# Performance work log

Measured on AMD Instinct MI355X. Metric: run time of the kernel, lower is better.

Reference implementation:

```python
import jax, jax.numpy as jnp
import numpy as np

B = 16; V = 30522; D = 512; H = 8; DH = 64; FF = 2048
NC = 4; NF = 30; NN = 34; FL = 64; HL = 32; NLAYERS = 2

def _pos_encoding(L, d):
    pos = np.arange(L)[:, None].astype(np.float32)
    i = np.arange(0, d, 2)[None, :].astype(np.float32)
    ang = pos / np.power(10000.0, i / d)
    pe = np.zeros((L, d), dtype=np.float32)
    pe[:, 0::2] = np.sin(ang)
    pe[:, 1::2] = np.cos(ang)
    return jnp.asarray(pe)

def _ln(x, g, b):
    m = x.mean(-1, keepdims=True)
    v = ((x - m) ** 2).mean(-1, keepdims=True)
    return (x - m) / jnp.sqrt(v + 1e-5) * g + b

def _encoder(ids, emb, Wqkv, bqkv, Wo, bo, ln1_g, ln1_b, Wff1, bff1, Wff2, bff2, ln2_g, ln2_b):
    Bx, L = ids.shape
    x = emb[ids] * jnp.sqrt(jnp.float32(D)) + _pos_encoding(L, D)
    for l in range(NLAYERS):  # torch post-norm encoder layer, relu FFN
        qkv = x @ Wqkv[l] + bqkv[l]
        q, k, v = jnp.split(qkv, 3, axis=-1)
        q = q.reshape(Bx, L, H, DH); k = k.reshape(Bx, L, H, DH); v = v.reshape(Bx, L, H, DH)
        att = jax.nn.softmax(jnp.einsum('blhd,bmhd->bhlm', q, k) / jnp.sqrt(jnp.float32(DH)), axis=-1)
        o = jnp.einsum('bhlm,bmhd->blhd', att, v).reshape(Bx, L, D) @ Wo[l] + bo[l]
        x = _ln(x + o, ln1_g[l], ln1_b[l])
        f = jax.nn.relu(x @ Wff1[l] + bff1[l]) @ Wff2[l] + bff2[l]
        x = _ln(x + f, ln2_g[l], ln2_b[l])
    return x

def _masked_mean(emb, mask):
    m = mask[..., None]
    return (emb * m).sum(1) / jnp.clip(m.sum(1), 1e-9, None)

def _solve_edges(W, adj, iters=100, lr=0.05, c=10.0):
    # differentiable proxy for the CvxpyLayer SDP relaxation: projected gradient
    # ascent on symmetric E in [0,1], maximizing sum(W*E) with quadratic penalties
    # for sum(adj*E) <= 6 and trace(E[:4,:4]) == 1 (PSD constraint dropped).
    diag4 = jnp.zeros((NN, NN)).at[jnp.arange(NC), jnp.arange(NC)].set(1.0)
    E0 = jnp.full(W.shape, 0.5)
    def step(E, _):
        s = jnp.sum(adj * E, axis=(1, 2), keepdims=True)
        d = jnp.sum(E * diag4, axis=(1, 2), keepdims=True)
        g = W - 2.0 * c * jax.nn.relu(s - 6.0) * adj - 2.0 * c * (d - 1.0) * diag4
        En = E + lr * g
        En = jnp.clip(0.5 * (En + jnp.swapaxes(En, 1, 2)), 0.0, 1.0)
        return En, None
    E, _ = jax.lax.scan(step, E0, None, length=iters)
    return E

def setup_inputs():
    key = jax.random.key(0)
    ks = jax.random.split(key, 24)
    w = lambda k, shape: (jax.random.normal(k, shape) * 0.02).astype(jnp.float32)
    return {
        'hypothesis_input_ids': jax.random.randint(ks[0], (B, NC, HL), 0, V),
        'hypothesis_attention_mask': jnp.ones((B, NC, HL), jnp.float32),
        'fact_attention_mask': jnp.ones((B, NF, FL), jnp.float32),
        'fact_input_ids': jax.random.randint(ks[1], (B, NF, FL), 0, V),
        'grounding_grounding_overlap': jax.random.uniform(ks[2], (B, NN, NN)),
        'abstract_abstract_overlap': jax.random.uniform(ks[3], (B, NN, NN)),
        'abstract_abstract_similarity': jax.random.uniform(ks[4], (B, NN, NN)),
        'question_grounding_overlap': jax.random.uniform(ks[5], (B, NN, NN)),
        'question_abstract_overlap': jax.random.uniform(ks[6], (B, NN, NN)),
        'question_abstract_similarity': jax.random.uniform(ks[7], (B, NN, NN)),
        'grounding_abstract_overlap': jax.random.uniform(ks[8], (B, NN, NN)),
        'question_question_score': w(ks[9], (B, NN, NN)),
        'labels': jax.random.randint(ks[10], (B,), 0, NC),
        'gold_similarity_scores': jax.random.normal(ks[11], (B, NC, NF)),
        'emb_table': w(ks[12], (V, D)),
        'Wqkv': w(ks[13], (NLAYERS, D, 3 * D)), 'bqkv': jnp.zeros((NLAYERS, 3 * D)),
        'Wo': w(ks[14], (NLAYERS, D, D)), 'bo': jnp.zeros((NLAYERS, D)),
        'ln1_g': jnp.ones((NLAYERS, D)), 'ln1_b': jnp.zeros((NLAYERS, D)),
        'Wff1': w(ks[15], (NLAYERS, D, FF)), 'bff1': jnp.zeros((NLAYERS, FF)),
        'Wff2': w(ks[16], (NLAYERS, FF, D)), 'bff2': jnp.zeros((NLAYERS, D)),
        'ln2_g': jnp.ones((NLAYERS, D)), 'ln2_b': jnp.zeros((NLAYERS, D)),
        'score_W': w(ks[17], (4 * D,)), 'score_b': jnp.zeros(()),
        'abs_score_W': w(ks[18], (4 * D,)), 'abs_score_b': jnp.zeros(()),
        'p_aa_overlap': jnp.ones(()), 'p_aa_sim': jnp.ones(()),
        'p_qa_overlap': jnp.ones(()), 'p_qa_sim': jnp.ones(()),
    }

def reference(hypothesis_input_ids, hypothesis_attention_mask, fact_attention_mask, fact_input_ids,
              grounding_grounding_overlap, abstract_abstract_overlap, abstract_abstract_similarity,
              question_grounding_overlap, question_abstract_overlap, question_abstract_similarity,
              grounding_abstract_overlap, question_question_score, labels, gold_similarity_scores,
              emb_table, Wqkv, bqkv, Wo, bo, ln1_g, ln1_b, Wff1, bff1, Wff2, bff2, ln2_g, ln2_b,
              score_W, score_b, abs_score_W, abs_score_b, p_aa_overlap, p_aa_sim, p_qa_overlap, p_qa_sim):
    enc = lambda ids: _encoder(ids, emb_table, Wqkv, bqkv, Wo, bo, ln1_g, ln1_b,
                               Wff1, bff1, Wff2, bff2, ln2_g, ln2_b)
    fseq = _masked_mean(enc(fact_input_ids.reshape(-1, FL)),
                        fact_attention_mask.reshape(-1, FL)).reshape(-1, NF, D)
    hseq = _masked_mean(enc(hypothesis_input_ids.reshape(-1, HL)),
                        hypothesis_attention_mask.reshape(-1, HL)).reshape(-1, NC, D)
    # abstract-abstract pairwise: concat(f_j, f_i, |f_j-f_i|, f_j*f_i) @ abs_score_W, done chunk-wise
    A1, A2, A3, A4 = jnp.split(abs_score_W, 4)
    aa = (fseq @ A1)[:, None, :] + (fseq @ A2)[:, :, None] \
       + jnp.einsum('bijd,d->bij', jnp.abs(fseq[:, None, :, :] - fseq[:, :, None, :]), A3) \
       + jnp.einsum('bid,bjd->bij', fseq * A4, fseq) + abs_score_b
    aa_sm = jax.nn.softmax(aa.reshape(-1, NF * NF), axis=1).reshape(-1, NF, NF)
    aa_sm = aa_sm * (1.0 - jnp.eye(NF))  # zero diagonal
    aa_sim = abstract_abstract_similarity.at[:, NC:, NC:].set(aa_sm)
    # question-abstract pairwise: concat(f_k, h_c, |f_k-h_c|, f_k*h_c) @ score_W
    S1, S2, S3, S4 = jnp.split(score_W, 4)
    qa = (fseq @ S1)[:, None, :] + (hseq @ S2)[:, :, None] \
       + jnp.einsum('bckd,d->bck', jnp.abs(fseq[:, None, :, :] - hseq[:, :, None, :]), S3) \
       + jnp.einsum('bkd,bcd->bck', fseq * S4, hseq) + score_b
    similarity_scores = jax.nn.softmax(qa, axis=2)  # [B, NC, NF]
    qa_sim = jnp.zeros_like(grounding_abstract_overlap)
    qa_sim = qa_sim.at[:, NC:, :NC].set(jnp.transpose(similarity_scores, (0, 2, 1)))
    qa_sim = qa_sim.at[:, :NC, NC:].set(similarity_scores)
    edge_weights = (-p_aa_overlap * abstract_abstract_overlap + p_aa_sim * aa_sim
                    + p_qa_overlap * question_abstract_overlap + p_qa_sim * qa_sim
                    + question_question_score)
    adj = (edge_weights != 0).astype(jnp.float32)
    edges = _solve_edges(edge_weights, adj)
    final_pred = jnp.diagonal(edges[:, :NC, :NC], axis1=1, axis2=2)  # [B, NC]
    gold = jax.nn.softmax(gold_similarity_scores, axis=2)
    logp = jax.nn.log_softmax(final_pred, axis=1)
    ce = -jnp.mean(logp[jnp.arange(final_pred.shape[0]), labels])
    mse = jnp.mean((similarity_scores - gold) ** 2)
    return ce + mse, final_pred
```

## Files before the change

kernel.cpp:

```cpp
#include <hip/hip_runtime.h>
#include <cstdint>
#include <cstddef>


using u16 = unsigned short;

typedef __bf16 bf16x8 __attribute__((ext_vector_type(8)));
typedef float  floatx4 __attribute__((ext_vector_type(4)));

#if defined(__has_builtin)
#if __has_builtin(__builtin_amdgcn_global_load_lds)
#define USE_GLL 1
#endif
#endif

__device__ __forceinline__ float bf2f(u16 u) {
  return __uint_as_float(((unsigned)u) << 16);
}
__device__ __forceinline__ u16 f2bf(float f) {
  unsigned u = __float_as_uint(f);
  u += 0x7FFFu + ((u >> 16) & 1u);
  return (u16)(u >> 16);
}
__device__ __forceinline__ float ldf(const void* p, size_t i, int isb) {
  return isb ? bf2f(((const u16*)p)[i]) : ((const float*)p)[i];
}

__device__ __forceinline__ float waveSum(float v) {
#pragma unroll
  for (int o = 32; o > 0; o >>= 1) v += __shfl_xor(v, o, 64);
  return v;
}
__device__ __forceinline__ float waveMax(float v) {
#pragma unroll
  for (int o = 32; o > 0; o >>= 1) v = fmaxf(v, __shfl_xor(v, o, 64));
  return v;
}
__device__ __forceinline__ float blockSum(float v, float* sh4) {
  v = waveSum(v);
  if ((threadIdx.x & 63) == 0) sh4[threadIdx.x >> 6] = v;
  __syncthreads();
  float r = sh4[0] + sh4[1] + sh4[2] + sh4[3];
  __syncthreads();
  return r;
}
__device__ __forceinline__ float blockMax(float v, float* sh4) {
  v = waveMax(v);
  if ((threadIdx.x & 63) == 0) sh4[threadIdx.x >> 6] = v;
  __syncthreads();
  float r = fmaxf(fmaxf(sh4[0], sh4[1]), fmaxf(sh4[2], sh4[3]));
  __syncthreads();
  return r;
}

__global__ void detect_kernel(const void* __restrict__ ln1g, int* __restrict__ flag) {
  unsigned u = *(const unsigned*)ln1g;
  *flag = (u == 0x3F800000u) ? 0 : 1;
}

__global__ __launch_bounds__(256) void pe_kernel(float* __restrict__ petab) {
  const int pos = blockIdx.x;
  const float LOG1E4_OVER_D = 9.210340371976184f / 512.0f;
  for (int d = threadIdx.x; d < 512; d += 256) {
    int i2 = d & ~1;
    float ang = (float)pos * expf(-(float)i2 * LOG1E4_OVER_D);
    petab[pos * 512 + d] = (d & 1) ? cosf(ang) : sinf(ang);
  }
}

__global__ __launch_bounds__(256) void transpose_kernel(const void* __restrict__ src,
                                                        u16* __restrict__ dst,
                                                        int K, int N,
                                                        size_t srcz, size_t dstz,
                                                        const int* __restrict__ F) {
  const int isb = *F;
  __shared__ u16 tile[32][33];
  size_t eoff = (size_t)blockIdx.z * srcz;
  u16* d = dst + (size_t)blockIdx.z * dstz;
  int bx = blockIdx.x, by = blockIdx.y;
  int tx = threadIdx.x & 31, ty = threadIdx.x >> 5;
  for (int i = ty; i < 32; i += 8)
    tile[i][tx] = f2bf(ldf(src, eoff + (size_t)(by * 32 + i) * N + bx * 32 + tx, isb));
  __syncthreads();
  for (int i = ty; i < 32; i += 8)
    d[(size_t)(bx * 32 + i) * K + by * 32 + tx] = tile[tx][i];
}

__global__ __launch_bounds__(256) void embed_kernel(const int* __restrict__ ids,
                                                    const void* __restrict__ emb,
                                                    u16* __restrict__ x, int L,
                                                    const float* __restrict__ petab,
                                                    const int* __restrict__ F) {
  const int isb = *F;
  int tok = blockIdx.x;
  int pos = tok % L;
  int id = ids[tok];
  for (int d = threadIdx.x; d < 512; d += 256) {
    float e = ldf(emb, (size_t)id * 512 + d, isb) * 22.62741699796952f;
    x[(size_t)tok * 512 + d] = f2bf(e + petab[pos * 512 + d]);
  }
}

__global__ __launch_bounds__(256) void embed2_kernel(const int* __restrict__ fids,
                                                     const int* __restrict__ hids,
                                                     const void* __restrict__ emb,
                                                     u16* __restrict__ x,
                                                     const float* __restrict__ petab,
                                                     const int* __restrict__ F) {
  const int isb = *F;
  int tok = blockIdx.x;
  int id, pos;
  if (tok < 30720) { id = fids[tok]; pos = tok & 63; }
  else             { int t2 = tok - 30720; id = hids[t2]; pos = t2 & 31; }
  for (int d = threadIdx.x; d < 512; d += 256) {
    float e = ldf(emb, (size_t)id * 512 + d, isb) * 22.62741699796952f;
    x[(size_t)tok * 512 + d] = f2bf(e + petab[pos * 512 + d]);
  }
}

template <int RELU>
__global__ __launch_bounds__(256, 2) void gemm_bt(const u16* __restrict__ A,
                                                  const u16* __restrict__ Bt,
                                                  const void* __restrict__ bias,
                                                  u16* __restrict__ C,
                                                  int M, int N, int K, size_t boff,
                                                  const int* __restrict__ F) {
  const int isb = *F;
  __shared__ __align__(16) u16 As[128 * 64];
  __shared__ __align__(16) u16 Bs[128 * 64];
  const int tid = threadIdx.x;
  const int lane = tid & 63;
  const int wave = tid >> 6;
  const int wm = wave >> 1, wn = wave & 1;
  const int l15 = lane & 15, quad = lane >> 4;

  const int nwg = gridDim.x * gridDim.y;
  const int hw  = blockIdx.y * gridDim.x + blockIdx.x;
  int lg;
  if ((nwg & 7) == 0) {
    lg = (hw & 7) * (nwg >> 3) + (hw >> 3);
  } else {
    int q = nwg >> 3, r = nwg & 7;
    int xcd = hw & 7, j = hw >> 3;
    lg = (xcd < r ? xcd * (q + 1) : r * (q + 1) + (xcd - r) * q) + j;
  }
  const int bm = lg / gridDim.x;
  const int bn = lg - bm * gridDim.x;

  floatx4 acc[4][4];
#pragma unroll
  for (int i = 0; i < 4; i++)
#pragma unroll
    for (int j = 0; j < 4; j++) acc[i][j] = (floatx4){0.f, 0.f, 0.f, 0.f};

  const u16* Abase = A + (size_t)bm * 128 * K;
  const u16* Bbase = Bt + (size_t)bn * 128 * K;

  for (int kt = 0; kt < K; kt += 64) {
#pragma unroll
    for (int i = 0; i < 4; i++) {
      int c = i * 256 + tid;
      int row = c >> 3, p = c & 7;
      int col = (((p - row) & 7)) * 8;
      const u16* ga = &Abase[(size_t)row * K + kt + col];
      const u16* gb = &Bbase[(size_t)row * K + kt + col];
#ifdef USE_GLL
      __builtin_amdgcn_global_load_lds(
          (const __attribute__((address_space(1))) void*)ga,
          (__attribute__((address_space(3))) void*)&As[c * 8], 16, 0, 0);
      __builtin_amdgcn_global_load_lds(
          (const __attribute__((address_space(1))) void*)gb,
          (__attribute__((address_space(3))) void*)&Bs[c * 8], 16, 0, 0);
#else
      *(uint4*)&As[c * 8] = *(const uint4*)ga;
      *(uint4*)&Bs[c * 8] = *(const uint4*)gb;
#endif
    }
    __syncthreads();
#pragma unroll
    for (int ks = 0; ks < 2; ks++) {
      bf16x8 af[4], bfr[4];
#pragma unroll
      for (int mi = 0; mi < 4; mi++) {
        int ra = wm * 64 + mi * 16 + l15;
        int q = ks * 4 + quad;
        af[mi] = *(const bf16x8*)&As[ra * 64 + ((q + ra) & 7) * 8];
      }
#pragma unroll
      for (int ni = 0; ni < 4; ni++) {
        int rb = wn * 64 + ni * 16 + l15;
        int q = ks * 4 + quad;
        bfr[ni] = *(const bf16x8*)&Bs[rb * 64 + ((q + rb) & 7) * 8];
      }
#pragma unroll
      for (int mi = 0; mi < 4; mi++)
#pragma unroll
        for (int ni = 0; ni < 4; ni++)
          acc[mi][ni] = __builtin_amdgcn_mfma_f32_16x16x32_bf16(af[mi], bfr[ni], acc[mi][ni], 0, 0, 0);
    }
    __syncthreads();
  }

  float bv[4];
  const int gcb = bn * 128 + wn * 64 + l15;
#pragma unroll
  for (int ni = 0; ni < 4; ni++) bv[ni] = ldf(bias, boff + gcb + ni * 16, isb);
#pragma unroll
  for (int mi = 0; mi < 4; mi++) {
#pragma unroll
    for (int r = 0; r < 4; r++) {
      int grow = bm * 128 + wm * 64 + mi * 16 + quad * 4 + r;
      size_t rb = (size_t)grow * N + gcb;
#pragma unroll
      for (int ni = 0; ni < 4; ni++) {
        float v = acc[mi][ni][r] + bv[ni];
        if (RELU) v = fmaxf(v, 0.f);
        C[rb + ni * 16] = f2bf(v);
      }
    }
  }
}

__global__ __launch_bounds__(256) void attn_kernel(const u16* __restrict__ qkv,
                                                   u16* __restrict__ o, int L,
                                                   int nblk1,
                                                   const u16* __restrict__ qkv2,
                                                   u16* __restrict__ o2, int L2) {
  int bid = blockIdx.x;
  if (bid >= nblk1) { qkv = qkv2; o = o2; L = L2; bid -= nblk1; }
  const int h = bid & 7;
  const int s = bid >> 3;
  __shared__ __align__(16) u16 Qs[64 * 72];
  __shared__ __align__(16) u16 Ks[64 * 72];
  __shared__ __align__(16) u16 Vt[64 * 72];
  __shared__ float Ss[64 * 66];
  const int tid = threadIdx.x;
  const int lane = tid & 63;
  const int wave = tid >> 6;
  const int wm = wave >> 1, wn = wave & 1;
  const int l15 = lane & 15, quad = lane >> 4;
  const int base = s * L;

  for (int idx = tid; idx < 512; idx += 256) {
    int t = idx >> 3, d8 = (idx & 7) * 8;
    int rot = ((t >> 3) + (idx & 7)) & 7;
    if (t < L) {
      size_t g = (size_t)(base + t) * 1536 + h * 64 + d8;
      *(uint4*)&Qs[t * 72 + d8] = *(const uint4*)&qkv[g];
      *(uint4*)&Ks[t * 72 + d8] = *(const uint4*)&qkv[g + 512];
      u16 vv[8];
      *(uint4*)vv = *(const uint4*)&qkv[g + 1024];
#pragma unroll
      for (int i = 0; i < 8; i++) Vt[(d8 + i) * 72 + rot * 8 + (t & 7)] = vv[i];
    } else {
      uint4 z = {0u, 0u, 0u, 0u};
      *(uint4*)&Qs[t * 72 + d8] = z;
      *(uint4*)&Ks[t * 72 + d8] = z;
#pragma unroll
      for (int i = 0; i < 8; i++) Vt[(d8 + i) * 72 + rot * 8 + (t & 7)] = 0;
    }
  }
  __syncthreads();

  {
    floatx4 acc[2][2];
#pragma unroll
    for (int mi = 0; mi < 2; mi++)
#pragma unroll
      for (int ni = 0; ni < 2; ni++) acc[mi][ni] = (floatx4){0.f, 0.f, 0.f, 0.f};
#pragma unroll
    for (int ks = 0; ks < 2; ks++) {
      bf16x8 af[2], bfr[2];
#pragma unroll
      for (int mi = 0; mi < 2; mi++)
        af[mi] = *(const bf16x8*)&Qs[(wm * 32 + mi * 16 + l15) * 72 + ks * 32 + quad * 8];
#pragma unroll
      for (int ni = 0; ni < 2; ni++)
        bfr[ni] = *(const bf16x8*)&Ks[(wn * 32 + ni * 16 + l15) * 72 + ks * 32 + quad * 8];
#pragma unroll
      for (int mi = 0; mi < 2; mi++)
#pragma unroll
        for (int ni = 0; ni < 2; ni++)
          acc[mi][ni] = __builtin_amdgcn_mfma_f32_16x16x32_bf16(af[mi], bfr[ni], acc[mi][ni], 0, 0, 0);
    }
#pragma unroll
    for (int mi = 0; mi < 2; mi++)
#pragma unroll
      for (int ni = 0; ni < 2; ni++)
#pragma unroll
        for (int r = 0; r < 4; r++)
          Ss[(wm * 32 + mi * 16 + quad * 4 + r) * 66 + wn * 32 + ni * 16 + l15] =
              acc[mi][ni][r] * 0.125f;
  }
  __syncthreads();

  {
    int r = tid >> 2, sub = tid & 3;
    int j0 = sub * 16;
    float mx = -3.4e38f;
    if (r < L)
      for (int j = j0; j < j0 + 16; j++)
        if (j < L) mx = fmaxf(mx, Ss[r * 66 + j]);
    mx = fmaxf(mx, __shfl_xor(mx, 1, 64));
    mx = fmaxf(mx, __shfl_xor(mx, 2, 64));
    float sum = 0.f;
    if (r < L)
      for (int j = j0; j < j0 + 16; j++)
        if (j < L) { float e = expf(Ss[r * 66 + j] - mx); Ss[r * 66 + j] = e; sum += e; }
    sum += __shfl_xor(sum, 1, 64);
    sum += __shfl_xor(sum, 2, 64);
    float inv = 1.f / sum;
    if (r < L)
      for (int j = j0; j < j0 + 16; j++)
        Qs[r * 72 + j] = (j < L) ? f2bf(Ss[r * 66 + j] * inv) : (u16)0;
  }
  __syncthreads();

  {
    floatx4 acc[2][2];
#pragma unroll
    for (int mi = 0; mi < 2; mi++)
#pragma unroll
      for (int ni = 0; ni < 2; ni++) acc[mi][ni] = (floatx4){0.f, 0.f, 0.f, 0.f};
#pragma unroll
    for (int ks = 0; ks < 2; ks++) {
      bf16x8 af[2], bfr[2];
#pragma unroll
      for (int mi = 0; mi < 2; mi++)
        af[mi] = *(const bf16x8*)&Qs[(wm * 32 + mi * 16 + l15) * 72 + ks * 32 + quad * 8];
#pragma unroll
      for (int ni = 0; ni < 2; ni++) {
        int rb = wn * 32 + ni * 16 + l15;
        int p = ((ks * 4 + quad) + (rb >> 3)) & 7;
        bfr[ni] = *(const bf16x8*)&Vt[rb * 72 + p * 8];
      }
#pragma unroll
      for (int mi = 0; mi < 2; mi++)
#pragma unroll
        for (int ni = 0; ni < 2; ni++)
          acc[mi][ni] = __builtin_amdgcn_mfma_f32_16x16x32_bf16(af[mi], bfr[ni], acc[mi][ni], 0, 0, 0);
    }
#pragma unroll
    for (int mi = 0; mi < 2; mi++) {
#pragma unroll
      for (int r = 0; r < 4; r++) {
        int t = wm * 32 + mi * 16 + quad * 4 + r;
        if (t < L) {
#pragma unroll
          for (int ni = 0; ni < 2; ni++) {
            int d = wn * 32 + ni * 16 + l15;
            o[(size_t)(base + t) * 512 + h * 64 + d] = f2bf(acc[mi][ni][r]);
          }
        }
      }
    }
  }
}

__global__ __launch_bounds__(256) void add_ln_kernel(u16* __restrict__ x,
                                                     const u16* __restrict__ y,
                                                     const void* __restrict__ g,
                                                     const void* __restrict__ b,
                                                     size_t eoff,
                                                     const int* __restrict__ F) {
  const int isb = *F;
  const int row = blockIdx.x, tid = threadIdx.x;
  __shared__ float sh[4];
  size_t o0 = (size_t)row * 512 + tid * 2;
  unsigned xv = *(const unsigned*)&x[o0];
  unsigned yv = *(const unsigned*)&y[o0];
  float v0 = bf2f((u16)xv) + bf2f((u16)yv);
  float v1 = bf2f((u16)(xv >> 16)) + bf2f((u16)(yv >> 16));
  float mean = blockSum(v0 + v1, sh) * (1.f / 512.f);
  float d0 = v0 - mean, d1 = v1 - mean;
  float var = blockSum(d0 * d0 + d1 * d1, sh) * (1.f / 512.f);
  float rstd = rsqrtf(var + 1e-5f);
  float g0 = ldf(g, eoff + tid * 2, isb),     g1 = ldf(g, eoff + tid * 2 + 1, isb);
  float b0 = ldf(b, eoff + tid * 2, isb),     b1 = ldf(b, eoff + tid * 2 + 1, isb);
  unsigned r0 = f2bf(d0 * rstd * g0 + b0);
  unsigned r1 = f2bf(d1 * rstd * g1 + b1);
  *(unsigned*)&x[o0] = r0 | (r1 << 16);
}

__global__ __launch_bounds__(256) void pool_kernel(const u16* __restrict__ x,
                                                   const void* __restrict__ mask,
                                                   float* __restrict__ pooled, int L,
                                                   size_t moff,
                                                   const int* __restrict__ F) {
  const int isb = *F;
  const int s = blockIdx.x;
  float msum = 0.f;
  for (int t = 0; t < L; t++) msum += ldf(mask, moff + s * L + t, isb);
  float inv = 1.f / fmaxf(msum, 1e-9f);
  for (int d = threadIdx.x; d < 512; d += 256) {
    float acc = 0.f;
    for (int t = 0; t < L; t++)
      acc += bf2f(x[(size_t)(s * L + t) * 512 + d]) * ldf(mask, moff + s * L + t, isb);
    pooled[(size_t)s * 512 + d] = acc * inv;
  }
}

__global__ __launch_bounds__(256) void pool2_kernel(const u16* __restrict__ xf,
                                                    const void* __restrict__ fmask,
                                                    float* __restrict__ fpool,
                                                    const u16* __restrict__ xh,
                                                    const void* __restrict__ hmask,
                                                    float* __restrict__ hpool,
                                                    const int* __restrict__ F) {
  const int isb = *F;
  const u16* x; const void* mask; float* pooled; int L, s;
  if (blockIdx.x < 480) { x = xf; mask = fmask; pooled = fpool; L = 64; s = blockIdx.x; }
  else                  { x = xh; mask = hmask; pooled = hpool; L = 32; s = blockIdx.x - 480; }
  float msum = 0.f;
  for (int t = 0; t < L; t++) msum += ldf(mask, (size_t)s * L + t, isb);
  float inv = 1.f / fmaxf(msum, 1e-9f);
  for (int d = threadIdx.x; d < 512; d += 256) {
    float acc = 0.f;
    for (int t = 0; t < L; t++)
      acc += bf2f(x[(size_t)(s * L + t) * 512 + d]) * ldf(mask, (size_t)s * L + t, isb);
    pooled[(size_t)s * 512 + d] = acc * inv;
  }
}

__global__ __launch_bounds__(64) void pair2_kernel(const float* __restrict__ FS,
                                                   const float* __restrict__ HS,
                                                   const void* __restrict__ absW,
                                                   const void* __restrict__ absB,
                                                   const void* __restrict__ scW,
                                                   const void* __restrict__ scB,
                                                   float* __restrict__ AA,
                                                   float* __restrict__ QA,
                                                   const int* __restrict__ F) {
  const int isb = *F;
  int gid = blockIdx.x;
  const float *X, *Y; const void *Wv, *bs; float* outp; int NI, NJ;
  if (gid < 14400) { X = FS; Y = FS; Wv = absW; bs = absB; outp = AA; NI = 30; NJ = 30; }
  else { gid -= 14400; X = HS; Y = FS; Wv = scW; bs = scB; outp = QA; NI = 4; NJ = 30; }
  int j = gid % NJ;
  int t = gid / NJ;
  int i = t % NI;
  int b = t / NI;
  const float* xv = X + ((size_t)b * NI + i) * 512;
  const float* yv = Y + ((size_t)b * NJ + j) * 512;
  int l = threadIdx.x;
  float p = 0.f;
  for (int d = l; d < 512; d += 64) {
    float xi = xv[d], yj = yv[d];
    p += ldf(Wv, d, isb) * yj + ldf(Wv, 512 + d, isb) * xi +
         ldf(Wv, 1024 + d, isb) * fabsf(yj - xi) + ldf(Wv, 1536 + d, isb) * xi * yj;
  }
  p = waveSum(p);
  if (l == 0) outp[gid] = p + ldf(bs, 0, isb);
}

__global__ __launch_bounds__(256) void sm2_kernel(const float* __restrict__ aa,
                                                  float* __restrict__ aasm,
                                                  const float* __restrict__ qa,
                                                  float* __restrict__ sim) {
  __shared__ float sh[4];
  if (blockIdx.x < 16) {
    const int b = blockIdx.x;
    const float* src = aa + (size_t)b * 900;
    float* dst = aasm + (size_t)b * 900;
    int tid = threadIdx.x;
    float mx = -3.4e38f;
    for (int i = tid; i < 900; i += 256) mx = fmaxf(mx, src[i]);
    mx = blockMax(mx, sh);
    float sum = 0.f;
    for (int i = tid; i < 900; i += 256) sum += expf(src[i] - mx);
    sum = blockSum(sum, sh);
    float inv = 1.f / sum;
    for (int i = tid; i < 900; i += 256) {
      int r = i / 30, c = i - r * 30;
      dst[i] = (r == c) ? 0.f : expf(src[i] - mx) * inv;
    }
  } else {
    int g = (blockIdx.x - 16) * 4 + (threadIdx.x >> 6);
    int l = threadIdx.x & 63;
    float v = (l < 30) ? qa[(size_t)g * 30 + l] : -3.4e38f;
    float mx = waveMax(v);
    float e = (l < 30) ? expf(v - mx) : 0.f;
    float s = waveSum(e);
    if (l < 30) sim[(size_t)g * 30 + l] = e / s;
  }
}

__global__ __launch_bounds__(256) void edgew_kernel(const void* __restrict__ aaov,
                                                    const void* __restrict__ aasim_in,
                                                    const void* __restrict__ qaov,
                                                    const void* __restrict__ qq,
                                                    const float* __restrict__ aasm,
                                                    const float* __restrict__ sim,
                                                    const void* __restrict__ p1,
                                                    const void* __restrict__ p2,
                                                    const void* __restrict__ p3,
                                                    const void* __restrict__ p4,
                                                    float* __restrict__ Wout,
                                                    const int* __restrict__ F) {
  const int isb = *F;
  int e = blockIdx.x * 256 + threadIdx.x;
  if (e >= 16 * 1156) return;
  int b = e / 1156;
  int rem = e - b * 1156;
  int r = rem / 34, c = rem - r * 34;
  float aas;
  if (r >= 4 && c >= 4) aas = aasm[(size_t)b * 900 + (r - 4) * 30 + (c - 4)];
  else                  aas = ldf(aasim_in, e, isb);
  float qas = 0.f;
  if (r >= 4 && c < 4)      qas = sim[((size_t)b * 4 + c) * 30 + (r - 4)];
  else if (r < 4 && c >= 4) qas = sim[((size_t)b * 4 + r) * 30 + (c - 4)];
  float w = -ldf(p1, 0, isb) * ldf(aaov, e, isb) + ldf(p2, 0, isb) * aas +
            ldf(p3, 0, isb) * ldf(qaov, e, isb) + ldf(p4, 0, isb) * qas +
            ldf(qq, e, isb);
  Wout[e] = w;
}

__global__ __launch_bounds__(64) void solve_kernel(const float* __restrict__ Wmat,
                                                   float* __restrict__ pred,
                                                   float* __restrict__ outp) {
  const int b = blockIdx.x;
  const int lane = threadIdx.x;
  float E[19], Ws[19], As[19];
  bool dg[19];
#pragma unroll
  for (int k = 0; k < 19; k++) {
    int e = lane + (k << 6);
    if (e < 1156) {
      int r = e / 34, c = e - r * 34;
      float w1 = Wmat[(size_t)b * 1156 + e];
      float w2 = Wmat[(size_t)b * 1156 + c * 34 + r];
      Ws[k] = 0.5f * (w1 + w2);
      As[k] = 0.5f * (((w1 != 0.f) ? 1.f : 0.f) + ((w2 != 0.f) ? 1.f : 0.f));
      dg[k] = (r == c && r < 4);
      E[k] = 0.5f;
    } else {
      Ws[k] = 0.f; As[k] = 0.f; dg[k] = false; E[k] = 0.f;
    }
  }
  for (int it = 0; it < 100; it++) {
    float ps = 0.f;
#pragma unroll
    for (int k = 0; k < 19; k++) ps += As[k] * E[k];
    float s = waveSum(ps);
    float dd = __shfl(E[0], 0, 64) + __shfl(E[0], 35, 64) +
               __shfl(E[1], 6, 64) + __shfl(E[1], 41, 64);
    float coef_s = (s > 6.f) ? 20.f * (s - 6.f) : 0.f;
    float coef_d = 20.f * (dd - 1.f);
#pragma unroll
    for (int k = 0; k < 19; k++) {
      float g = Ws[k] - coef_s * As[k] - (dg[k] ? coef_d : 0.f);
      E[k] = fminf(fmaxf(E[k] + 0.05f * g, 0.f), 1.f);
    }
  }
  float v0 = E[0], v1 = E[1];
  if (lane == 0)  { pred[b * 4 + 0] = v0; outp[1 + b * 4 + 0] = v0; }
  if (lane == 35) { pred[b * 4 + 1] = v0; outp[1 + b * 4 + 1] = v0; }
  if (lane == 6)  { pred[b * 4 + 2] = v1; outp[1 + b * 4 + 2] = v1; }
  if (lane == 41) { pred[b * 4 + 3] = v1; outp[1 + b * 4 + 3] = v1; }
}

__global__ __launch_bounds__(256) void loss_kernel(const float* __restrict__ sim,
                                                   const void* __restrict__ gold,
                                                   const float* __restrict__ pred,
                                                   const int* __restrict__ labels,
                                                   float* __restrict__ outp,
                                                   const int* __restrict__ F) {
  const int isb = *F;
  __shared__ float sh[4];
  const int tid = threadIdx.x;
  float local = 0.f;
  if (tid < 64) {
    float mx = -3.4e38f;
    for (int k = 0; k < 30; k++) mx = fmaxf(mx, ldf(gold, (size_t)tid * 30 + k, isb));
    float sum = 0.f;
    for (int k = 0; k < 30; k++) sum += expf(ldf(gold, (size_t)tid * 30 + k, isb) - mx);
    float inv = 1.f / sum;
    for (int k = 0; k < 30; k++) {
      float gsm = expf(ldf(gold, (size_t)tid * 30 + k, isb) - mx) * inv;
      float d = sim[(size_t)tid * 30 + k] - gsm;
      local += d * d;
    }
  }
  float mse = blockSum(local, sh) * (1.f / 1920.f);
  float cel = 0.f;
  if (tid < 16) {
    const float* f = pred + tid * 4;
    int lb = labels[tid] & 3;
    float mx = fmaxf(fmaxf(f[0], f[1]), fmaxf(f[2], f[3]));
    float lse = logf(expf(f[0] - mx) + expf(f[1] - mx) + expf(f[2] - mx) + expf(f[3] - mx));
    float lp = f[lb] - mx - lse;
    cel = -lp * (1.f / 16.f);
  }
  float ce = blockSum(cel, sh);
  if (tid == 0) outp[0] = ce + mse;
}

extern "C" void kernel_launch(void* const* d_in, const int* in_sizes, int n_in,
                              void* d_out, int out_size, void* d_ws, size_t ws_size,
                              hipStream_t stream) {
  (void)in_sizes; (void)n_in; (void)out_size;
  const int*  hyp_ids   = (const int*)d_in[0];
  const void* hyp_mask  = d_in[1];
  const void* fact_mask = d_in[2];
  const int*  fact_ids  = (const int*)d_in[3];
  const void* aa_ov     = d_in[5];
  const void* aa_sim_in = d_in[6];
  const void* qa_ov     = d_in[8];
  const void* qq        = d_in[11];
  const int*  labels    = (const int*)d_in[12];
  const void* gold      = d_in[13];
  const void* emb       = d_in[14];
  const void* Wqkv      = d_in[15];
  const void* bqkv      = d_in[16];
  const void* Wo        = d_in[17];
  const void* bo        = d_in[18];
  const void* ln1g      = d_in[19];
  const void* ln1b      = d_in[20];
  const void* Wff1      = d_in[21];
  const void* bff1      = d_in[22];
  const void* Wff2      = d_in[23];
  const void* bff2      = d_in[24];
  const void* ln2g      = d_in[25];
  const void* ln2b      = d_in[26];
  const void* scoreW    = d_in[27];
  const void* scoreB    = d_in[28];
  const void* absW      = d_in[29];
  const void* absB      = d_in[30];
  const void* p_aaov    = d_in[31];
  const void* p_aasim   = d_in[32];
  const void* p_qaov    = d_in[33];
  const void* p_qasim   = d_in[34];
  float* out = (float*)d_out;

  char* ws = (char*)d_ws;
  size_t off = 0;
  auto alloc = [&](size_t bytes) -> void* {
    void* p = ws + off;
    off += (bytes + 255) & ~(size_t)255;
    return p;
  };

  float* PRED = (float*)alloc(64ull * 4);
  int*   FLAG = (int*)alloc(256);
  float* SIM  = (float*)alloc(16ull * 120 * 4);
  float* QA   = (float*)alloc(16ull * 120 * 4);
  float* AASM = (float*)alloc(16ull * 900 * 4);
  float* AA   = (float*)alloc(16ull * 900 * 4);
  float* WMAT = (float*)alloc(16ull * 1156 * 4);
  float* FSEQ = (float*)alloc(480ull * 512 * 4);
  float* HSEQ = (float*)alloc(64ull * 512 * 4);
  float* PETAB= (float*)alloc(64ull * 512 * 4);
  u16* WT_QKV = (u16*)alloc(2ull * 1536 * 512 * 2);
  u16* WT_O   = (u16*)alloc(2ull * 512 * 512 * 2);
  u16* WT_F1  = (u16*)alloc(2ull * 2048 * 512 * 2);
  u16* WT_F2  = (u16*)alloc(2ull * 512 * 2048 * 2);

  const int opts_tok[6] = {32768, 30720, 15360, 10240, 6144, 3072};
  const int opts_nch[6] = {1, 1, 2, 3, 5, 10};
  int CH_TOK = 3072, NCH = 10;
  for (int i = 0; i < 6; i++) {
    size_t need = off + (size_t)opts_tok[i] * 7168 + 4096;
    if (need <= ws_size) { CH_TOK = opts_tok[i]; NCH = opts_nch[i]; break; }
  }
  u16* X   = (u16*)alloc((size_t)CH_TOK * 512 * 2);
  u16* BIG = (u16*)alloc((size_t)CH_TOK * 2048 * 2);
  u16* ATT = (u16*)alloc((size_t)CH_TOK * 512 * 2);
  u16* Y   = (u16*)alloc((size_t)CH_TOK * 512 * 2);

  detect_kernel<<<1, 1, 0, stream>>>(ln1g, FLAG);
  pe_kernel<<<64, 256, 0, stream>>>(PETAB);

  transpose_kernel<<<dim3(48, 16, 2), 256, 0, stream>>>(
      Wqkv, WT_QKV, 512, 1536, 512ull * 1536, 1536ull * 512, FLAG);
  transpose_kernel<<<dim3(16, 16, 2), 256, 0, stream>>>(
      Wo, WT_O, 512, 512, 512ull * 512, 512ull * 512, FLAG);
  transpose_kernel<<<dim3(64, 16, 2), 256, 0, stream>>>(
      Wff1, WT_F1, 512, 2048, 512ull * 2048, 2048ull * 512, FLAG);
  transpose_kernel<<<dim3(16, 64, 2), 256, 0, stream>>>(
      Wff2, WT_F2, 2048, 512, 2048ull * 512, 512ull * 2048, FLAG);

  if (CH_TOK >= 32768) {
    const int M = 32768;
    const size_t HOFF = 30720;
    embed2_kernel<<<M, 256, 0, stream>>>(fact_ids, hyp_ids, emb, X, PETAB, FLAG);
    for (int l = 0; l < 2; l++) {
      gemm_bt<0><<<dim3(12, M / 128), 256, 0, stream>>>(
          X, WT_QKV + (size_t)l * 1536 * 512, bqkv, BIG, M, 1536, 512,
          (size_t)l * 1536, FLAG);
      attn_kernel<<<480 * 8 + 64 * 8, 256, 0, stream>>>(
          BIG, ATT, 64, 480 * 8, BIG + HOFF * 1536, ATT + HOFF * 512, 32);
      gemm_bt<0><<<dim3(4, M / 128), 256, 0, stream>>>(
          ATT, WT_O + (size_t)l * 512 * 512, bo, Y, M, 512, 512,
          (size_t)l * 512, FLAG);
      add_ln_kernel<<<M, 256, 0, stream>>>(X, Y, ln1g, ln1b, (size_t)l * 512, FLAG);
      gemm_bt<1><<<dim3(16, M / 128), 256, 0, stream>>>(
          X, WT_F1 + (size_t)l * 2048 * 512, bff1, BIG, M, 2048, 512,
          (size_t)l * 2048, FLAG);
      gemm_bt<0><<<dim3(4, M / 128), 256, 0, stream>>>(
          BIG, WT_F2 + (size_t)l * 512 * 2048, bff2, Y, M, 512, 2048,
          (size_t)l * 512, FLAG);
      add_ln_kernel<<<M, 256, 0, stream>>>(X, Y, ln2g, ln2b, (size_t)l * 512, FLAG);
    }
    pool2_kernel<<<544, 256, 0, stream>>>(X, fact_mask, FSEQ,
                                          X + HOFF * 512, hyp_mask, HSEQ, FLAG);
  } else {
    auto encode = [&](const int* ids, int nseq, int L, const void* mask,
                      size_t moff, float* pooled) {
      int M = nseq * L;
      embed_kernel<<<M, 256, 0, stream>>>(ids, emb, X, L, PETAB, FLAG);
      for (int l = 0; l < 2; l++) {
        gemm_bt<0><<<dim3(12, M / 128), 256, 0, stream>>>(
            X, WT_QKV + (size_t)l * 1536 * 512, bqkv, BIG, M, 1536, 512,
            (size_t)l * 1536, FLAG);
        attn_kernel<<<nseq * 8, 256, 0, stream>>>(BIG, ATT, L, nseq * 8, BIG, ATT, L);
        gemm_bt<0><<<dim3(4, M / 128), 256, 0, stream>>>(
            ATT, WT_O + (size_t)l * 512 * 512, bo, Y, M, 512, 512,
            (size_t)l * 512, FLAG);
        add_ln_kernel<<<M, 256, 0, stream>>>(X, Y, ln1g, ln1b, (size_t)l * 512, FLAG);
        gemm_bt<1><<<dim3(16, M / 128), 256, 0, stream>>>(
            X, WT_F1 + (size_t)l * 2048 * 512, bff1, BIG, M, 2048, 512,
            (size_t)l * 2048, FLAG);
        gemm_bt<0><<<dim3(4, M / 128), 256, 0, stream>>>(
            BIG, WT_F2 + (size_t)l * 512 * 2048, bff2, Y, M, 512, 2048,
            (size_t)l * 512, FLAG);
        add_ln_kernel<<<M, 256, 0, stream>>>(X, Y, ln2g, ln2b, (size_t)l * 512, FLAG);
      }
      pool_kernel<<<nseq, 256, 0, stream>>>(X, mask, pooled, L, moff, FLAG);
    };
    const int seq_per = 480 / NCH;
    for (int c = 0; c < NCH; c++) {
      encode(fact_ids + (size_t)c * seq_per * 64, seq_per, 64, fact_mask,
             (size_t)c * seq_per * 64, FSEQ + (size_t)c * seq_per * 512);
    }
    encode(hyp_ids, 64, 32, hyp_mask, 0, HSEQ);
  }

  pair2_kernel<<<16 * 30 * 30 + 16 * 4 * 30, 64, 0, stream>>>(
      FSEQ, HSEQ, absW, absB, scoreW, scoreB, AA, QA, FLAG);
  sm2_kernel<<<32, 256, 0, stream>>>(AA, AASM, QA, SIM);

  edgew_kernel<<<(16 * 1156 + 255) / 256, 256, 0, stream>>>(
      aa_ov, aa_sim_in, qa_ov, qq, AASM, SIM, p_aaov, p_aasim, p_qaov, p_qasim,
      WMAT, FLAG);
  solve_kernel<<<16, 64, 0, stream>>>(WMAT, PRED, out);
  loss_kernel<<<1, 256, 0, stream>>>(SIM, gold, PRED, labels, out, FLAG);
}
```

Baseline: 990.1 us.

## Fuse setup kernels into one launch and keep attention softmax in registers

Merges the dtype detect, positional-encoding, and four weight-transpose launches into a single setup kernel that dispatches on block index, cutting five kernel launches. In the attention kernel, softmax is now computed directly on the MFMA accumulators using cross-lane shuffles plus small shared row-stat arrays. This replaces the round trip through a float score buffer in shared memory. The change lowers LDS traffic and footprint, which may raise occupancy, at the cost of two extra block barriers and more live registers.

```diff
diff --git a/kernel.cpp b/kernel.cpp
--- a/kernel.cpp
+++ b/kernel.cpp
@@ -53,31 +53,51 @@
   return r;
 }
 
-__global__ void detect_kernel(const void* __restrict__ ln1g, int* __restrict__ flag) {
-  unsigned u = *(const unsigned*)ln1g;
-  *flag = (u == 0x3F800000u) ? 0 : 1;
-}
-
-__global__ __launch_bounds__(256) void pe_kernel(float* __restrict__ petab) {
-  const int pos = blockIdx.x;
-  const float LOG1E4_OVER_D = 9.210340371976184f / 512.0f;
-  for (int d = threadIdx.x; d < 512; d += 256) {
-    int i2 = d & ~1;
-    float ang = (float)pos * expf(-(float)i2 * LOG1E4_OVER_D);
-    petab[pos * 512 + d] = (d & 1) ? cosf(ang) : sinf(ang);
-  }
-}
-
-__global__ __launch_bounds__(256) void transpose_kernel(const void* __restrict__ src,
-                                                        u16* __restrict__ dst,
-                                                        int K, int N,
-                                                        size_t srcz, size_t dstz,
-                                                        const int* __restrict__ F) {
-  const int isb = *F;
+__global__ __launch_bounds__(256) void setup_kernel(const void* __restrict__ Wqkv,
+                                                    const void* __restrict__ Wo,
+                                                    const void* __restrict__ Wff1,
+                                                    const void* __restrict__ Wff2,
+                                                    u16* __restrict__ WT_QKV,
+                                                    u16* __restrict__ WT_O,
+                                                    u16* __restrict__ WT_F1,
+                                                    u16* __restrict__ WT_F2,
+                                                    float* __restrict__ petab,
+                                                    const void* __restrict__ ln1g,
+                                                    int* __restrict__ flag) {
+  const int bid = blockIdx.x;
+  unsigned u0 = *(const unsigned*)ln1g;
+  const int isb = (u0 == 0x3F800000u) ? 0 : 1;
+  if (bid == 0 && threadIdx.x == 0) *flag = isb;
+
+  if (bid >= 6144) {
+    int pos = bid - 6144;
+    const float LOG1E4_OVER_D = 9.210340371976184f / 512.0f;
+    for (int d = threadIdx.x; d < 512; d += 256) {
+      int i2 = d & ~1;
+      float ang = (float)pos * expf(-(float)i2 * LOG1E4_OVER_D);
+      petab[pos * 512 + d] = (d & 1) ? cosf(ang) : sinf(ang);
+    }
+    return;
+  }
+
+  const void* src; u16* dst; int K, N, bx, by, z;
+  if (bid < 1536) {
+    src = Wqkv; dst = WT_QKV; K = 512; N = 1536;
+    z = bid / 768; int r = bid % 768; bx = r % 48; by = r / 48;
+  } else if (bid < 2048) {
+    src = Wo; dst = WT_O; K = 512; N = 512;
+    int t = bid - 1536; z = t / 256; int r = t % 256; bx = r % 16; by = r / 16;
+  } else if (bid < 4096) {
+    src = Wff1; dst = WT_F1; K = 512; N = 2048;
+    int t = bid - 2048; z = t / 1024; int r = t % 1024; bx = r % 64; by = r / 64;
+  } else {
+    src = Wff2; dst = WT_F2; K = 2048; N = 512;
+    int t = bid - 4096; z = t / 1024; int r = t % 1024; bx = r % 16; by = r / 16;
+  }
+  size_t plane = (size_t)K * N;
+  size_t eoff = (size_t)z * plane;
+  u16* d = dst + (size_t)z * plane;
   __shared__ u16 tile[32][33];
-  size_t eoff = (size_t)blockIdx.z * srcz;
-  u16* d = dst + (size_t)blockIdx.z * dstz;
-  int bx = blockIdx.x, by = blockIdx.y;
   int tx = threadIdx.x & 31, ty = threadIdx.x >> 5;
   for (int i = ty; i < 32; i += 8)
     tile[i][tx] = f2bf(ldf(src, eoff + (size_t)(by * 32 + i) * N + bx * 32 + tx, isb));
@@ -233,7 +253,8 @@
   __shared__ __align__(16) u16 Qs[64 * 72];
   __shared__ __align__(16) u16 Ks[64 * 72];
   __shared__ __align__(16) u16 Vt[64 * 72];
-  __shared__ float Ss[64 * 66];
+  __shared__ float rstatM[64][2];
+  __shared__ float rstatS[64][2];
   const int tid = threadIdx.x;
   const int lane = tid & 63;
   const int wave = tid >> 6;
@@ -262,57 +283,100 @@
   }
   __syncthreads();
 
+  floatx4 sacc[2][2];
+#pragma unroll
+  for (int mi = 0; mi < 2; mi++)
+#pragma unroll
+    for (int ni = 0; ni < 2; ni++) sacc[mi][ni] = (floatx4){0.f, 0.f, 0.f, 0.f};
+#pragma unroll
+  for (int ks = 0; ks < 2; ks++) {
+    bf16x8 af[2], bfr[2];
+#pragma unroll
+    for (int mi = 0; mi < 2; mi++)
+      af[mi] = *(const bf16x8*)&Qs[(wm * 32 + mi * 16 + l15) * 72 + ks * 32 + quad * 8];
+#pragma unroll
+    for (int ni = 0; ni < 2; ni++)
+      bfr[ni] = *(const bf16x8*)&Ks[(wn * 32 + ni * 16 + l15) * 72 + ks * 32 + quad * 8];
+#pragma unroll
+    for (int mi = 0; mi < 2; mi++)
+#pragma unroll
+      for (int ni = 0; ni < 2; ni++)
+        sacc[mi][ni] = __builtin_amdgcn_mfma_f32_16x16x32_bf16(af[mi], bfr[ni], sacc[mi][ni], 0, 0, 0);
+  }
+
   {
-    floatx4 acc[2][2];
+    const int c0ok = (wn * 32 + l15) < L;
+    const int c1ok = (wn * 32 + 16 + l15) < L;
+    float pm[2][4];
 #pragma unroll
     for (int mi = 0; mi < 2; mi++)
 #pragma unroll
-      for (int ni = 0; ni < 2; ni++) acc[mi][ni] = (floatx4){0.f, 0.f, 0.f, 0.f};
-#pragma unroll
-    for (int ks = 0; ks < 2; ks++) {
-      bf16x8 af[2], bfr[2];
+      for (int r = 0; r < 4; r++) {
+        float a = c0ok ? sacc[mi][0][r] * 0.125f : -3.4e38f;
+        float c = c1ok ? sacc[mi][1][r] * 0.125f : -3.4e38f;
+        pm[mi][r] = fmaxf(a, c);
+      }
+#pragma unroll
+    for (int off = 1; off <= 8; off <<= 1)
 #pragma unroll
       for (int mi = 0; mi < 2; mi++)
-        af[mi] = *(const bf16x8*)&Qs[(wm * 32 + mi * 16 + l15) * 72 + ks * 32 + quad * 8];
-#pragma unroll
-      for (int ni = 0; ni < 2; ni++)
-        bfr[ni] = *(const bf16x8*)&Ks[(wn * 32 + ni * 16 + l15) * 72 + ks * 32 + quad * 8];
+#pragma unroll
+        for (int r = 0; r < 4; r++)
+          pm[mi][r] = fmaxf(pm[mi][r], __shfl_xor(pm[mi][r], off, 64));
+    if (l15 == 0) {
 #pragma unroll
       for (int mi = 0; mi < 2; mi++)
 #pragma unroll
+        for (int r = 0; r < 4; r++)
+          rstatM[wm * 32 + mi * 16 + quad * 4 + r][wn] = pm[mi][r];
+    }
+    __syncthreads();
+
+    float mx[2][4];
+#pragma unroll
+    for (int mi = 0; mi < 2; mi++)
+#pragma unroll
+      for (int r = 0; r < 4; r++) {
+        int row = wm * 32 + mi * 16 + quad * 4 + r;
+        mx[mi][r] = fmaxf(rstatM[row][0], rstatM[row][1]);
+      }
+    float ev[2][2][4];
+    float ps[2][4];
+#pragma unroll
+    for (int mi = 0; mi < 2; mi++)
+#pragma unroll
+      for (int r = 0; r < 4; r++) {
+        float e0 = c0ok ? expf(sacc[mi][0][r] * 0.125f - mx[mi][r]) : 0.f;
+        float e1 = c1ok ? expf(sacc[mi][1][r] * 0.125f - mx[mi][r]) : 0.f;
+        ev[mi][0][r] = e0; ev[mi][1][r] = e1;
+        ps[mi][r] = e0 + e1;
+      }
+#pragma unroll
+    for (int off = 1; off <= 8; off <<= 1)
+#pragma unroll
+      for (int mi = 0; mi < 2; mi++)
+#pragma unroll
+        for (int r = 0; r < 4; r++)
+          ps[mi][r] += __shfl_xor(ps[mi][r], off, 64);
+    if (l15 == 0) {
+#pragma unroll
+      for (int mi = 0; mi < 2; mi++)
+#pragma unroll
+        for (int r = 0; r < 4; r++)
+          rstatS[wm * 32 + mi * 16 + quad * 4 + r][wn] = ps[mi][r];
+    }
+    __syncthreads();
+
+#pragma unroll
+    for (int mi = 0; mi < 2; mi++)
+#pragma unroll
+      for (int r = 0; r < 4; r++) {
+        int row = wm * 32 + mi * 16 + quad * 4 + r;
+        float inv = 1.f / (rstatS[row][0] + rstatS[row][1]);
+#pragma unroll
         for (int ni = 0; ni < 2; ni++)
-          acc[mi][ni] = __builtin_amdgcn_mfma_f32_16x16x32_bf16(af[mi], bfr[ni], acc[mi][ni], 0, 0, 0);
-    }
-#pragma unroll
-    for (int mi = 0; mi < 2; mi++)
-#pragma unroll
-      for (int ni = 0; ni < 2; ni++)
-#pragma unroll
-        for (int r = 0; r < 4; r++)
-          Ss[(wm * 32 + mi * 16 + quad * 4 + r) * 66 + wn * 32 + ni * 16 + l15] =
-              acc[mi][ni][r] * 0.125f;
-  }
-  __syncthreads();
-
-  {
-    int r = tid >> 2, sub = tid & 3;
-    int j0 = sub * 16;
-    float mx = -3.4e38f;
-    if (r < L)
-      for (int j = j0; j < j0 + 16; j++)
-        if (j < L) mx = fmaxf(mx, Ss[r * 66 + j]);
-    mx = fmaxf(mx, __shfl_xor(mx, 1, 64));
-    mx = fmaxf(mx, __shfl_xor(mx, 2, 64));
-    float sum = 0.f;
-    if (r < L)
-      for (int j = j0; j < j0 + 16; j++)
-        if (j < L) { float e = expf(Ss[r * 66 + j] - mx); Ss[r * 66 + j] = e; sum += e; }
-    sum += __shfl_xor(sum, 1, 64);
-    sum += __shfl_xor(sum, 2, 64);
-    float inv = 1.f / sum;
-    if (r < L)
-      for (int j = j0; j < j0 + 16; j++)
-        Qs[r * 72 + j] = (j < L) ? f2bf(Ss[r * 66 + j] * inv) : (u16)0;
+          Qs[row * 72 + wn * 32 + ni * 16 + l15] = f2bf(ev[mi][ni][r] * inv);
+      }
   }
   __syncthreads();
 
@@ -667,17 +731,9 @@
   u16* ATT = (u16*)alloc((size_t)CH_TOK * 512 * 2);
   u16* Y   = (u16*)alloc((size_t)CH_TOK * 512 * 2);
 
-  detect_kernel<<<1, 1, 0, stream>>>(ln1g, FLAG);
-  pe_kernel<<<64, 256, 0, stream>>>(PETAB);
-
-  transpose_kernel<<<dim3(48, 16, 2), 256, 0, stream>>>(
-      Wqkv, WT_QKV, 512, 1536, 512ull * 1536, 1536ull * 512, FLAG);
-  transpose_kernel<<<dim3(16, 16, 2), 256, 0, stream>>>(
-      Wo, WT_O, 512, 512, 512ull * 512, 512ull * 512, FLAG);
-  transpose_kernel<<<dim3(64, 16, 2), 256, 0, stream>>>(
-      Wff1, WT_F1, 512, 2048, 512ull * 2048, 2048ull * 512, FLAG);
-  transpose_kernel<<<dim3(16, 64, 2), 256, 0, stream>>>(
-      Wff2, WT_F2, 2048, 512, 2048ull * 512, 512ull * 2048, FLAG);
+  setup_kernel<<<6208, 256, 0, stream>>>(Wqkv, Wo, Wff1, Wff2,
+                                         WT_QKV, WT_O, WT_F1, WT_F2,
+                                         PETAB, ln1g, FLAG);
 
   if (CH_TOK >= 32768) {
     const int M = 32768;
```

Measured after the change: 951.5 us. 3.9% less time.
